# Kernel optimization log

Measured on AMD Instinct MI355X. Metric: run time of the kernel, lower is better.

## Reference

```python
import jax, jax.numpy as jnp
import numpy as np

B, L1, L2 = 4, 512, 512
K1D, K2D, V1D, V2D, A = 256, 256, 256, 256, 128


def setup_inputs() -> dict:
    key = jax.random.key(0)
    ks = jax.random.split(key, 12)
    n = lambda i, shape, sc=1.0: (jax.random.normal(ks[i], shape, jnp.float32) * sc)
    return {
        "k1": n(0, (B, L1, K1D)),
        "k2": n(1, (B, L2, K2D)),
        "v1": n(2, (B, L1, V1D)),
        "v2": n(3, (B, L2, V2D)),
        "W1": n(4, (K1D, A), 0.05),
        "b1": n(5, (A,), 0.05),
        "W2": n(6, (K2D, A), 0.05),
        "b2": n(7, (A,), 0.05),
        "ws": n(8, (A,), 0.05),
        "bs": n(9, (), 0.05),
        # lengths in [L/2, L) so every softmax row has at least one finite entry
        "k1_lengths": jax.random.randint(ks[10], (B,), L1 // 2, L1, dtype=jnp.int32),
        "k2_lengths": jax.random.randint(ks[11], (B,), L2 // 2, L2, dtype=jnp.int32),
    }


def reference(k1, k2, v1, v2, W1, b1, W2, b2, ws, bs, k1_lengths, k2_lengths):
    # projected keys: [B,L1,A], [B,L2,A]
    p1 = jnp.einsum("bik,ka->bia", k1, W1) + b1
    p2 = jnp.einsum("bjk,ka->bja", k2, W2) + b2
    h = jnp.tanh(p1[:, :, None, :] + p2[:, None, :, :])  # [B,L1,L2,A]
    score = jnp.einsum("bija,a->bij", h, ws) + bs
    # torch mask semantics: +1 for padded k1 rows, +1 for padded k2 cols, mask where sum == 1
    row_pad = (jnp.arange(L1)[None, :] >= k1_lengths[:, None]).astype(jnp.int32)  # [B,L1]
    col_pad = (jnp.arange(L2)[None, :] >= k2_lengths[:, None]).astype(jnp.int32)  # [B,L2]
    mask = (row_pad[:, :, None] + col_pad[:, None, :]) == 1  # [B,L1,L2]
    score = jnp.where(mask, -jnp.inf, score)
    w1 = jax.nn.softmax(jnp.transpose(score, (0, 2, 1)), axis=-1)  # [B,L2,L1], softmax over L1
    w2 = jax.nn.softmax(score, axis=-1)                             # [B,L1,L2], softmax over L2
    o1 = jnp.matmul(w1, v1)  # [B,L2,V1D]
    o2 = jnp.matmul(w2, v2)  # [B,L1,V2D]
    return (o1, o2, w1, w2, score)
```

## Files before the change

kernel.cpp:

```cpp
#include <hip/hip_runtime.h>
#include <math.h>

#define NB 4
#define NL1 512
#define NL2 512
#define NKD 256
#define NA 128
#define NV 256

#define O1_OFF 0
#define O2_OFF (NB*NL2*NV)
#define W1_OFF (O2_OFF + NB*NL1*NV)
#define W2_OFF (W1_OFF + NB*NL2*NL1)
#define SC_OFF (W2_OFF + NB*NL1*NL2)

#define MASK_NEG (-1e30f)

#define SC2LOG2E 2.8853900817779268f

#if __has_builtin(__builtin_amdgcn_exp2f)
#define EXP2F(x) __builtin_amdgcn_exp2f(x)
#else
#define EXP2F(x) __expf((x) * 0.6931471805599453f)
#endif
#if __has_builtin(__builtin_amdgcn_rcpf)
#define RCPF(x) __builtin_amdgcn_rcpf(x)
#else
#define RCPF(x) (1.0f / (x))
#endif

__global__ __launch_bounds__(128) void proj_kernel(
    const float* __restrict__ k1, const float* __restrict__ k2,
    const float* __restrict__ W1, const float* __restrict__ b1,
    const float* __restrict__ W2, const float* __restrict__ b2,
    float* __restrict__ p1, float* __restrict__ p2)
{
    __shared__ float kr[4][NKD];
    int blk = blockIdx.x;
    int tid = threadIdx.x;
    const float *K, *W, *bias; float* P; int rowbase;
    if (blk < (NB*NL1)/4) { K = k1; W = W1; bias = b1; P = p1; rowbase = blk*4; }
    else                  { K = k2; W = W2; bias = b2; P = p2; rowbase = (blk - (NB*NL1)/4)*4; }
    for (int idx = tid; idx < 256; idx += 128) {
        int r = idx >> 6, c = idx & 63;
        *(float4*)&kr[r][c*4] = *(const float4*)&K[(rowbase + r)*NKD + c*4];
    }
    __syncthreads();
    int a = tid;
    float acc0 = bias[a], acc1 = bias[a], acc2 = bias[a], acc3 = bias[a];
    #pragma unroll 4
    for (int k = 0; k < NKD; k++) {
        float wv = W[k*NA + a];
        acc0 = fmaf(kr[0][k], wv, acc0);
        acc1 = fmaf(kr[1][k], wv, acc1);
        acc2 = fmaf(kr[2][k], wv, acc2);
        acc3 = fmaf(kr[3][k], wv, acc3);
    }
    P[(rowbase+0)*NA + a] = acc0 * SC2LOG2E;
    P[(rowbase+1)*NA + a] = acc1 * SC2LOG2E;
    P[(rowbase+2)*NA + a] = acc2 * SC2LOG2E;
    P[(rowbase+3)*NA + a] = acc3 * SC2LOG2E;
}

#define P1_STRIDE 132
#define P2_STRIDE 36

#define TERM(acc, wv, xv, yv) acc = fmaf((wv), RCPF(1.0f + EXP2F((xv)+(yv))), (acc))

__global__ __launch_bounds__(256) void score_kernel(
    const float* __restrict__ p1, const float* __restrict__ p2,
    const float* __restrict__ ws, const float* __restrict__ bs,
    const int* __restrict__ len1, const int* __restrict__ len2,
    float* __restrict__ score, float* __restrict__ w1pre)
{
    __shared__ float p1t[32][P1_STRIDE];
    __shared__ float p2t[NA][P2_STRIDE];
    __shared__ float wst[NA];
    __shared__ float wsum[2];
    __shared__ float tile[32][33];
    int b  = blockIdx.z;
    int i0 = blockIdx.y * 32, j0 = blockIdx.x * 32;
    int tid = threadIdx.x;
    if (tid < 128) {
        float w = ws[tid];
        wst[tid] = -2.0f * w;
        float v = w;
        #pragma unroll
        for (int o = 32; o > 0; o >>= 1) v += __shfl_xor(v, o);
        if ((tid & 63) == 0) wsum[tid >> 6] = v;
    }
    const float* p1src = p1 + (b*NL1 + i0)*NA;
    const float* p2src = p2 + (b*NL2 + j0)*NA;
    for (int idx = tid; idx < 1024; idx += 256) {
        int r = idx >> 5, c = idx & 31;
        *(float4*)&p1t[r][c*4] = *(const float4*)&p1src[r*NA + c*4];
    }
    for (int idx = tid; idx < 1024; idx += 256) {
        int j = idx >> 5, c = idx & 31;
        float4 t = *(const float4*)&p2src[j*NA + c*4];
        p2t[c*4+0][j] = t.x; p2t[c*4+1][j] = t.y;
        p2t[c*4+2][j] = t.z; p2t[c*4+3][j] = t.w;
    }
    __syncthreads();

    int tx = tid & 15, ty = tid >> 4;
    int il = ty*2, jl = tx*2;
    float acc00 = 0.f, acc01 = 0.f, acc10 = 0.f, acc11 = 0.f;
    #pragma unroll 4
    for (int a = 0; a < NA; a += 2) {
        float2 wv = *(float2*)&wst[a];
        float2 x0 = *(float2*)&p1t[il  ][a];
        float2 x1 = *(float2*)&p1t[il+1][a];
        float2 y0 = *(float2*)&p2t[a  ][jl];
        float2 y1 = *(float2*)&p2t[a+1][jl];
        TERM(acc00, wv.x, x0.x, y0.x); TERM(acc00, wv.y, x0.y, y1.x);
        TERM(acc01, wv.x, x0.x, y0.y); TERM(acc01, wv.y, x0.y, y1.y);
        TERM(acc10, wv.x, x1.x, y0.x); TERM(acc10, wv.y, x1.y, y1.x);
        TERM(acc11, wv.x, x1.x, y0.y); TERM(acc11, wv.y, x1.y, y1.y);
    }
    float sb = wsum[0] + wsum[1] + bs[0];
    int n1 = len1[b], n2 = len2[b];
    float accs[2][2] = {{acc00, acc01}, {acc10, acc11}};
    #pragma unroll
    for (int di = 0; di < 2; di++) {
        #pragma unroll
        for (int dj = 0; dj < 2; dj++) {
            int gi = i0 + il + di, gj = j0 + jl + dj;
            float v = accs[di][dj] + sb;
            int rp = (gi >= n1), cp = (gj >= n2);
            if (rp + cp == 1) v = MASK_NEG;
            score[(b*NL1 + gi)*NL2 + gj] = v;
            tile[il + di][jl + dj] = v;
        }
    }
    __syncthreads();
    #pragma unroll
    for (int di = 0; di < 2; di++) {
        int rr = il + di;
        float2 t = make_float2(tile[jl][rr], tile[jl+1][rr]);
        *(float2*)&w1pre[((size_t)b*NL2 + j0 + rr)*NL1 + i0 + jl] = t;
    }
}

__device__ __forceinline__ float wave_max(float v) {
    #pragma unroll
    for (int o = 32; o > 0; o >>= 1) v = fmaxf(v, __shfl_xor(v, o));
    return v;
}
__device__ __forceinline__ float wave_sum(float v) {
    #pragma unroll
    for (int o = 32; o > 0; o >>= 1) v += __shfl_xor(v, o);
    return v;
}

__global__ __launch_bounds__(256) void softmax_both(const float* __restrict__ score,
                                                    float* __restrict__ w2,
                                                    float* __restrict__ w1)
{
    __shared__ float sm[4], ss[4];
    int row = blockIdx.x, tid = threadIdx.x;
    const float* s; float* d;
    if (row < NB*NL1) { s = score + (size_t)row * NL2; d = w2 + (size_t)row * NL2; }
    else { size_t r = row - NB*NL1; s = w1 + r * NL1; d = w1 + r * NL1; }
    float x0 = s[tid], x1 = s[tid + 256];
    float m = wave_max(fmaxf(x0, x1));
    if ((tid & 63) == 0) sm[tid >> 6] = m;
    __syncthreads();
    m = fmaxf(fmaxf(sm[0], sm[1]), fmaxf(sm[2], sm[3]));
    float e0 = __expf(x0 - m), e1 = __expf(x1 - m);
    float sum = wave_sum(e0 + e1);
    if ((tid & 63) == 0) ss[tid >> 6] = sum;
    __syncthreads();
    sum = (ss[0] + ss[1]) + (ss[2] + ss[3]);
    float inv = 1.0f / sum;
    d[tid] = e0 * inv; d[tid + 256] = e1 * inv;
}

typedef __attribute__((ext_vector_type(8))) short bf16x8;
typedef __attribute__((ext_vector_type(4))) float f32x4;

__device__ __forceinline__ unsigned short f2bf(float f) {
    unsigned u = __float_as_uint(f);
    u += 0x7fffu + ((u >> 16) & 1u);
    return (unsigned short)(u >> 16);
}

#define VT_STRIDE 520

__global__ __launch_bounds__(256) void out_matmul(
    const float* __restrict__ w2m, const float* __restrict__ w1m,
    const float* __restrict__ v2,  const float* __restrict__ v1,
    float* __restrict__ o2, float* __restrict__ o1)
{
    __shared__ unsigned short Wt[64 * VT_STRIDE];
    __shared__ unsigned short Vt[64 * VT_STRIDE];
    int z = blockIdx.z; int b = z >> 1, m = z & 1;
    const float* Wm = (m ? w1m : w2m) + (size_t)b * NL1 * NL2;
    const float* Vm = (m ? v1 : v2)   + (size_t)b * NL2 * NV;
    float*       Om = (m ? o1 : o2)   + (size_t)b * NL1 * NV;
    int r0 = blockIdx.y * 64, d0 = blockIdx.x * 64;
    int tid = threadIdx.x;
    int lane = tid & 63, wid = tid >> 6;
    int wy = wid >> 1, wx = wid & 1;
    int lm = lane & 15, kg = lane >> 4;

    {
        int wr = tid >> 5;
        int wc = tid & 31;
        #pragma unroll
        for (int p = 0; p < 8; p++) {
            int r = wr + 8 * p;
            const float* src = Wm + (size_t)(r0 + r) * 512;
            unsigned short* dstrow = &Wt[r * VT_STRIDE];
            #pragma unroll
            for (int k = 0; k < 4; k++) {
                int s = 4 * (wc + 32 * k);
                float4 f = *(const float4*)&src[s];
                unsigned lo = (unsigned)f2bf(f.x) | ((unsigned)f2bf(f.y) << 16);
                unsigned hi = (unsigned)f2bf(f.z) | ((unsigned)f2bf(f.w) << 16);
                *(unsigned*)&dstrow[s]     = lo;
                *(unsigned*)&dstrow[s + 2] = hi;
            }
        }
    }
    {
        int tm = tid & 15, tg = tid >> 4;
        #pragma unroll 4
        for (int u = 0; u < 16; u++) {
            int s = 2 * tg + 32 * u;
            #pragma unroll
            for (int j = 0; j < 4; j++) {
                int d = tm + 16 * j;
                float f0 = Vm[(size_t)s * NV + d0 + d];
                float f1 = Vm[(size_t)(s + 1) * NV + d0 + d];
                unsigned pk = (unsigned)f2bf(f0) | ((unsigned)f2bf(f1) << 16);
                *(unsigned*)&Vt[d * VT_STRIDE + s] = pk;
            }
        }
    }
    __syncthreads();

    const unsigned short* Wlo = &Wt[(wy * 32 + lm) * VT_STRIDE];
    const unsigned short* Whi = Wlo + 16 * VT_STRIDE;
    const unsigned short* Vlo = &Vt[(wx * 32 + lm) * VT_STRIDE];
    const unsigned short* Vhi = Vlo + 16 * VT_STRIDE;

    f32x4 acc00 = {0.f,0.f,0.f,0.f}, acc01 = {0.f,0.f,0.f,0.f};
    f32x4 acc10 = {0.f,0.f,0.f,0.f}, acc11 = {0.f,0.f,0.f,0.f};
    #pragma unroll 4
    for (int t = 0; t < 16; t++) {
        int s0 = t * 32 + 8 * kg;
        bf16x8 fa0 = *(const bf16x8*)(Wlo + s0);
        bf16x8 fa1 = *(const bf16x8*)(Whi + s0);
        bf16x8 fb0 = *(const bf16x8*)(Vlo + s0);
        bf16x8 fb1 = *(const bf16x8*)(Vhi + s0);
        acc00 = __builtin_amdgcn_mfma_f32_16x16x32_bf16(fa0, fb0, acc00, 0, 0, 0);
        acc01 = __builtin_amdgcn_mfma_f32_16x16x32_bf16(fa0, fb1, acc01, 0, 0, 0);
        acc10 = __builtin_amdgcn_mfma_f32_16x16x32_bf16(fa1, fb0, acc10, 0, 0, 0);
        acc11 = __builtin_amdgcn_mfma_f32_16x16x32_bf16(fa1, fb1, acc11, 0, 0, 0);
    }

    int rlo = r0 + wy * 32 + 4 * kg;
    int clo = d0 + wx * 32 + lm;
    #pragma unroll
    for (int e = 0; e < 4; e++) {
        Om[(size_t)(rlo + e) * NV + clo]           = acc00[e];
        Om[(size_t)(rlo + e) * NV + clo + 16]      = acc01[e];
        Om[(size_t)(rlo + 16 + e) * NV + clo]      = acc10[e];
        Om[(size_t)(rlo + 16 + e) * NV + clo + 16] = acc11[e];
    }
}

extern "C" void kernel_launch(void* const* d_in, const int* in_sizes, int n_in,
                              void* d_out, int out_size, void* d_ws, size_t ws_size,
                              hipStream_t stream) {
    const float* k1  = (const float*)d_in[0];
    const float* k2  = (const float*)d_in[1];
    const float* v1  = (const float*)d_in[2];
    const float* v2  = (const float*)d_in[3];
    const float* W1  = (const float*)d_in[4];
    const float* b1  = (const float*)d_in[5];
    const float* W2  = (const float*)d_in[6];
    const float* b2  = (const float*)d_in[7];
    const float* wsv = (const float*)d_in[8];
    const float* bsp = (const float*)d_in[9];
    const int* len1  = (const int*)d_in[10];
    const int* len2  = (const int*)d_in[11];

    float* out   = (float*)d_out;
    float* o1    = out + O1_OFF;
    float* o2    = out + O2_OFF;
    float* w1    = out + W1_OFF;
    float* w2    = out + W2_OFF;
    float* score = out + SC_OFF;

    float* p1    = (float*)d_ws;
    float* p2    = p1 + NB*NL1*NA;

    proj_kernel<<<dim3((NB*NL1)/4 + (NB*NL2)/4), 128, 0, stream>>>(k1, k2, W1, b1, W2, b2, p1, p2);
    score_kernel<<<dim3(NL2/32, NL1/32, NB), 256, 0, stream>>>(p1, p2, wsv, bsp, len1, len2, score, w1);
    softmax_both<<<dim3(NB*NL1 + NB*NL2), 256, 0, stream>>>(score, w2, w1);
    out_matmul<<<dim3(NV/64, NL1/64, NB*2), 256, 0, stream>>>(w2, w1, v2, v1, o2, o1);
}
```

Before: 72.67 us.

## Use one wave per softmax row, K-split matmul staging, widen score loads

The softmax kernel now handles four rows per block, one wavefront per row, with float4 loads and shuffle-only reductions. This removes the shared-memory reductions and block barriers. The output matmul stages its K dimension in two halves of 256, which cuts shared memory per block so more blocks can be resident, at the cost of an extra barrier and reload phase. The score kernel's inner loop reads p1 and ws as float4 and processes four A elements per iteration, reducing LDS load instructions.

```diff
diff --git a/kernel.cpp b/kernel.cpp
--- a/kernel.cpp
+++ b/kernel.cpp
@@ -106,17 +106,23 @@
     int tx = tid & 15, ty = tid >> 4;
     int il = ty*2, jl = tx*2;
     float acc00 = 0.f, acc01 = 0.f, acc10 = 0.f, acc11 = 0.f;
-    #pragma unroll 4
-    for (int a = 0; a < NA; a += 2) {
-        float2 wv = *(float2*)&wst[a];
-        float2 x0 = *(float2*)&p1t[il  ][a];
-        float2 x1 = *(float2*)&p1t[il+1][a];
+    #pragma unroll 2
+    for (int a = 0; a < NA; a += 4) {
+        float4 wv = *(float4*)&wst[a];
+        float4 x0 = *(float4*)&p1t[il  ][a];
+        float4 x1 = *(float4*)&p1t[il+1][a];
         float2 y0 = *(float2*)&p2t[a  ][jl];
         float2 y1 = *(float2*)&p2t[a+1][jl];
-        TERM(acc00, wv.x, x0.x, y0.x); TERM(acc00, wv.y, x0.y, y1.x);
-        TERM(acc01, wv.x, x0.x, y0.y); TERM(acc01, wv.y, x0.y, y1.y);
-        TERM(acc10, wv.x, x1.x, y0.x); TERM(acc10, wv.y, x1.y, y1.x);
-        TERM(acc11, wv.x, x1.x, y0.y); TERM(acc11, wv.y, x1.y, y1.y);
+        float2 y2 = *(float2*)&p2t[a+2][jl];
+        float2 y3 = *(float2*)&p2t[a+3][jl];
+        TERM(acc00, wv.x, x0.x, y0.x); TERM(acc01, wv.x, x0.x, y0.y);
+        TERM(acc10, wv.x, x1.x, y0.x); TERM(acc11, wv.x, x1.x, y0.y);
+        TERM(acc00, wv.y, x0.y, y1.x); TERM(acc01, wv.y, x0.y, y1.y);
+        TERM(acc10, wv.y, x1.y, y1.x); TERM(acc11, wv.y, x1.y, y1.y);
+        TERM(acc00, wv.z, x0.z, y2.x); TERM(acc01, wv.z, x0.z, y2.y);
+        TERM(acc10, wv.z, x1.z, y2.x); TERM(acc11, wv.z, x1.z, y2.y);
+        TERM(acc00, wv.w, x0.w, y3.x); TERM(acc01, wv.w, x0.w, y3.y);
+        TERM(acc10, wv.w, x1.w, y3.x); TERM(acc11, wv.w, x1.w, y3.y);
     }
     float sb = wsum[0] + wsum[1] + bs[0];
     int n1 = len1[b], n2 = len2[b];
@@ -142,38 +148,34 @@
     }
 }
 
-__device__ __forceinline__ float wave_max(float v) {
-    #pragma unroll
-    for (int o = 32; o > 0; o >>= 1) v = fmaxf(v, __shfl_xor(v, o));
-    return v;
-}
-__device__ __forceinline__ float wave_sum(float v) {
-    #pragma unroll
-    for (int o = 32; o > 0; o >>= 1) v += __shfl_xor(v, o);
-    return v;
-}
-
 __global__ __launch_bounds__(256) void softmax_both(const float* __restrict__ score,
                                                     float* __restrict__ w2,
                                                     float* __restrict__ w1)
 {
-    __shared__ float sm[4], ss[4];
-    int row = blockIdx.x, tid = threadIdx.x;
+    int row = blockIdx.x * 4 + (threadIdx.x >> 6);
+    int lane = threadIdx.x & 63;
     const float* s; float* d;
     if (row < NB*NL1) { s = score + (size_t)row * NL2; d = w2 + (size_t)row * NL2; }
     else { size_t r = row - NB*NL1; s = w1 + r * NL1; d = w1 + r * NL1; }
-    float x0 = s[tid], x1 = s[tid + 256];
-    float m = wave_max(fmaxf(x0, x1));
-    if ((tid & 63) == 0) sm[tid >> 6] = m;
-    __syncthreads();
-    m = fmaxf(fmaxf(sm[0], sm[1]), fmaxf(sm[2], sm[3]));
-    float e0 = __expf(x0 - m), e1 = __expf(x1 - m);
-    float sum = wave_sum(e0 + e1);
-    if ((tid & 63) == 0) ss[tid >> 6] = sum;
-    __syncthreads();
-    sum = (ss[0] + ss[1]) + (ss[2] + ss[3]);
+    float4 v0 = *(const float4*)&s[lane * 4];
+    float4 v1 = *(const float4*)&s[256 + lane * 4];
+    float m = fmaxf(fmaxf(fmaxf(v0.x, v0.y), fmaxf(v0.z, v0.w)),
+                    fmaxf(fmaxf(v1.x, v1.y), fmaxf(v1.z, v1.w)));
+    #pragma unroll
+    for (int o = 32; o > 0; o >>= 1) m = fmaxf(m, __shfl_xor(m, o));
+    float4 e0, e1;
+    e0.x = __expf(v0.x - m); e0.y = __expf(v0.y - m);
+    e0.z = __expf(v0.z - m); e0.w = __expf(v0.w - m);
+    e1.x = __expf(v1.x - m); e1.y = __expf(v1.y - m);
+    e1.z = __expf(v1.z - m); e1.w = __expf(v1.w - m);
+    float sum = (e0.x + e0.y) + (e0.z + e0.w) + (e1.x + e1.y) + (e1.z + e1.w);
+    #pragma unroll
+    for (int o = 32; o > 0; o >>= 1) sum += __shfl_xor(sum, o);
     float inv = 1.0f / sum;
-    d[tid] = e0 * inv; d[tid + 256] = e1 * inv;
+    e0.x *= inv; e0.y *= inv; e0.z *= inv; e0.w *= inv;
+    e1.x *= inv; e1.y *= inv; e1.z *= inv; e1.w *= inv;
+    *(float4*)&d[lane * 4] = e0;
+    *(float4*)&d[256 + lane * 4] = e1;
 }
 
 typedef __attribute__((ext_vector_type(8))) short bf16x8;
@@ -184,16 +186,19 @@
     u += 0x7fffu + ((u >> 16) & 1u);
     return (unsigned short)(u >> 16);
 }
-
-#define VT_STRIDE 520
+__device__ __forceinline__ unsigned pk2bf(float a, float b) {
+    return (unsigned)f2bf(a) | ((unsigned)f2bf(b) << 16);
+}
+
+#define KT 264
 
 __global__ __launch_bounds__(256) void out_matmul(
     const float* __restrict__ w2m, const float* __restrict__ w1m,
     const float* __restrict__ v2,  const float* __restrict__ v1,
     float* __restrict__ o2, float* __restrict__ o1)
 {
-    __shared__ unsigned short Wt[64 * VT_STRIDE];
-    __shared__ unsigned short Vt[64 * VT_STRIDE];
+    __shared__ unsigned short Wt[64 * KT];
+    __shared__ unsigned short Vt[64 * KT];
     int z = blockIdx.z; int b = z >> 1, m = z & 1;
     const float* Wm = (m ? w1m : w2m) + (size_t)b * NL1 * NL2;
     const float* Vm = (m ? v1 : v2)   + (size_t)b * NL2 * NV;
@@ -204,60 +209,60 @@
     int wy = wid >> 1, wx = wid & 1;
     int lm = lane & 15, kg = lane >> 4;
 
-    {
-        int wr = tid >> 5;
-        int wc = tid & 31;
-        #pragma unroll
-        for (int p = 0; p < 8; p++) {
-            int r = wr + 8 * p;
-            const float* src = Wm + (size_t)(r0 + r) * 512;
-            unsigned short* dstrow = &Wt[r * VT_STRIDE];
+    const unsigned short* Wlo = &Wt[(wy * 32 + lm) * KT];
+    const unsigned short* Whi = Wlo + 16 * KT;
+    const unsigned short* Vlo = &Vt[(wx * 32 + lm) * KT];
+    const unsigned short* Vhi = Vlo + 16 * KT;
+
+    f32x4 acc00 = {0.f,0.f,0.f,0.f}, acc01 = {0.f,0.f,0.f,0.f};
+    f32x4 acc10 = {0.f,0.f,0.f,0.f}, acc11 = {0.f,0.f,0.f,0.f};
+
+    for (int h = 0; h < 2; h++) {
+        if (h) __syncthreads();
+        int sbase = h * 256;
+        {
+            int wr = tid >> 5, wc = tid & 31;
             #pragma unroll
-            for (int k = 0; k < 4; k++) {
-                int s = 4 * (wc + 32 * k);
-                float4 f = *(const float4*)&src[s];
-                unsigned lo = (unsigned)f2bf(f.x) | ((unsigned)f2bf(f.y) << 16);
-                unsigned hi = (unsigned)f2bf(f.z) | ((unsigned)f2bf(f.w) << 16);
-                *(unsigned*)&dstrow[s]     = lo;
-                *(unsigned*)&dstrow[s + 2] = hi;
+            for (int p = 0; p < 8; p++) {
+                int r = wr + 8 * p;
+                const float* src = Wm + (size_t)(r0 + r) * 512 + sbase;
+                unsigned short* dstrow = &Wt[r * KT];
+                #pragma unroll
+                for (int k = 0; k < 2; k++) {
+                    int s = 4 * (wc + 32 * k);
+                    float4 f = *(const float4*)&src[s];
+                    *(unsigned*)&dstrow[s]     = pk2bf(f.x, f.y);
+                    *(unsigned*)&dstrow[s + 2] = pk2bf(f.z, f.w);
+                }
             }
         }
-    }
-    {
-        int tm = tid & 15, tg = tid >> 4;
-        #pragma unroll 4
-        for (int u = 0; u < 16; u++) {
-            int s = 2 * tg + 32 * u;
-            #pragma unroll
-            for (int j = 0; j < 4; j++) {
-                int d = tm + 16 * j;
-                float f0 = Vm[(size_t)s * NV + d0 + d];
-                float f1 = Vm[(size_t)(s + 1) * NV + d0 + d];
-                unsigned pk = (unsigned)f2bf(f0) | ((unsigned)f2bf(f1) << 16);
-                *(unsigned*)&Vt[d * VT_STRIDE + s] = pk;
+        {
+            int tm = tid & 15, tg = tid >> 4;
+            #pragma unroll 4
+            for (int u = 0; u < 8; u++) {
+                int s = 2 * tg + 32 * u;
+                #pragma unroll
+                for (int j = 0; j < 4; j++) {
+                    int d = tm + 16 * j;
+                    float f0 = Vm[(size_t)(sbase + s) * NV + d0 + d];
+                    float f1 = Vm[(size_t)(sbase + s + 1) * NV + d0 + d];
+                    *(unsigned*)&Vt[d * KT + s] = pk2bf(f0, f1);
+                }
             }
         }
-    }
-    __syncthreads();
-
-    const unsigned short* Wlo = &Wt[(wy * 32 + lm) * VT_STRIDE];
-    const unsigned short* Whi = Wlo + 16 * VT_STRIDE;
-    const unsigned short* Vlo = &Vt[(wx * 32 + lm) * VT_STRIDE];
-    const unsigned short* Vhi = Vlo + 16 * VT_STRIDE;
-
-    f32x4 acc00 = {0.f,0.f,0.f,0.f}, acc01 = {0.f,0.f,0.f,0.f};
-    f32x4 acc10 = {0.f,0.f,0.f,0.f}, acc11 = {0.f,0.f,0.f,0.f};
-    #pragma unroll 4
-    for (int t = 0; t < 16; t++) {
-        int s0 = t * 32 + 8 * kg;
-        bf16x8 fa0 = *(const bf16x8*)(Wlo + s0);
-        bf16x8 fa1 = *(const bf16x8*)(Whi + s0);
-        bf16x8 fb0 = *(const bf16x8*)(Vlo + s0);
-        bf16x8 fb1 = *(const bf16x8*)(Vhi + s0);
-        acc00 = __builtin_amdgcn_mfma_f32_16x16x32_bf16(fa0, fb0, acc00, 0, 0, 0);
-        acc01 = __builtin_amdgcn_mfma_f32_16x16x32_bf16(fa0, fb1, acc01, 0, 0, 0);
-        acc10 = __builtin_amdgcn_mfma_f32_16x16x32_bf16(fa1, fb0, acc10, 0, 0, 0);
-        acc11 = __builtin_amdgcn_mfma_f32_16x16x32_bf16(fa1, fb1, acc11, 0, 0, 0);
+        __syncthreads();
+        #pragma unroll 4
+        for (int t = 0; t < 8; t++) {
+            int s0 = t * 32 + 8 * kg;
+            bf16x8 fa0 = *(const bf16x8*)(Wlo + s0);
+            bf16x8 fa1 = *(const bf16x8*)(Whi + s0);
+            bf16x8 fb0 = *(const bf16x8*)(Vlo + s0);
+            bf16x8 fb1 = *(const bf16x8*)(Vhi + s0);
+            acc00 = __builtin_amdgcn_mfma_f32_16x16x32_bf16(fa0, fb0, acc00, 0, 0, 0);
+            acc01 = __builtin_amdgcn_mfma_f32_16x16x32_bf16(fa0, fb1, acc01, 0, 0, 0);
+            acc10 = __builtin_amdgcn_mfma_f32_16x16x32_bf16(fa1, fb0, acc10, 0, 0, 0);
+            acc11 = __builtin_amdgcn_mfma_f32_16x16x32_bf16(fa1, fb1, acc11, 0, 0, 0);
+        }
     }
 
     int rlo = r0 + wy * 32 + 4 * kg;
@@ -299,6 +304,6 @@
 
     proj_kernel<<<dim3((NB*NL1)/4 + (NB*NL2)/4), 128, 0, stream>>>(k1, k2, W1, b1, W2, b2, p1, p2);
     score_kernel<<<dim3(NL2/32, NL1/32, NB), 256, 0, stream>>>(p1, p2, wsv, bsp, len1, len2, score, w1);
-    softmax_both<<<dim3(NB*NL1 + NB*NL2), 256, 0, stream>>>(score, w2, w1);
+    softmax_both<<<dim3((NB*NL1 + NB*NL2)/4), 256, 0, stream>>>(score, w2, w1);
     out_matmul<<<dim3(NV/64, NL1/64, NB*2), 256, 0, stream>>>(w2, w1, v2, v1, o2, o1);
 }
```

Result: no change. 71.85 us (-1.1%).
